# Kernel tuning notes

Measured on AMD Instinct MI355X. Metric: run time of the kernel, lower is better.

The kernel has to match this reference:

```python
import math
import jax, jax.numpy as jnp
import numpy as np

TOP_K = 16
LOW_FREQ = 1
MAX_SEL = 32


def setup_inputs() -> dict:
    key = jax.random.key(0)
    x = jax.random.normal(key, (32, 2048, 512), dtype=jnp.float32)
    return {"x": x}


def reference(x):
    # x: (B, T, D)
    B, T, D = x.shape
    dtype = x.dtype

    xf = jnp.fft.rfft(x, axis=1)  # (B, T//2+1, D) complex
    f_full = jnp.fft.rfftfreq(T, d=1.0).astype(dtype)
    if T % 2 == 0:
        xf = xf[:, LOW_FREQ:-1, :]
        f_vec = f_full[LOW_FREQ:-1]
    else:
        xf = xf[:, LOW_FREQ:, :]
        f_vec = f_full[LOW_FREQ:]
    Lf = xf.shape[1]
    K = min(TOP_K, Lf)

    # top-k over frequency axis, per (b, d)
    xf_t = jnp.transpose(xf, (0, 2, 1))  # (B, D, Lf)
    _, idx = jax.lax.top_k(jnp.abs(xf_t), K)  # (B, D, K), sorted descending
    idx = idx[:, :, : min(MAX_SEL, K)]
    Ksel = idx.shape[2]

    x_sel = jnp.take_along_axis(xf_t, idx, axis=2)  # (B, D, Ksel) complex
    f_sel = f_vec[idx]                               # (B, D, Ksel)
    amp = jnp.abs(x_sel).astype(dtype)
    ph = jnp.angle(x_sel).astype(dtype)

    # y[b,t,d] = sum_k amp * cos(2*pi*f*t + phase), t = linspace(0,1,T)
    two_pi_t = (2.0 * math.pi) * jnp.linspace(0.0, 1.0, T, dtype=dtype)  # (T,)

    def step(acc, kin):
        a, f, p = kin  # each (B, D)
        acc = acc + a[..., None] * jnp.cos(f[..., None] * two_pi_t + p[..., None])
        return acc, None

    init = jnp.zeros((B, D, T), dtype)
    ks = (jnp.moveaxis(amp, 2, 0), jnp.moveaxis(f_sel, 2, 0), jnp.moveaxis(ph, 2, 0))
    y_bdt, _ = jax.lax.scan(step, init, ks)
    return jnp.transpose(y_bdt, (0, 2, 1))  # (B, T, D)
```

## Files before the change

kernel.cpp:

```cpp
#include <hip/hip_runtime.h>
#include <math.h>

#ifndef M_PI
#define M_PI 3.14159265358979323846
#endif

constexpr int cB = 32;
constexpr int cT = 2048;
constexpr int cD = 512;
constexpr int cK = 16;
constexpr int TCH = 64;

__device__ __forceinline__ int PZ(int i) { return i + (i >> 4); }

__device__ __forceinline__ float2 twLO(const float2* TW, int e) {
  return TW[PZ(e)];
}
__device__ __forceinline__ float2 twHI(const float2* TW, int e) {
  float2 w = TW[PZ(e - 512)];
  return make_float2(w.y, -w.x);
}
__device__ __forceinline__ float2 twDYN(const float2* TW, int e) {
  float2 w = TW[PZ(e & 511)];
  return (e < 512) ? w : make_float2(w.y, -w.x);
}

__global__ __launch_bounds__(256) void k_transpose(const float* __restrict__ x,
                                                   float* __restrict__ xt) {
  __shared__ float tile[64][65];
  const int b  = blockIdx.z;
  const int t0 = blockIdx.y * 64;
  const int d0 = blockIdx.x * 64;
  const int tid = threadIdx.x;
  const int r = tid >> 4;
  const int c = tid & 15;

  const float4* x4 = (const float4*)(x + ((size_t)b * cT + t0) * cD + d0);
#pragma unroll
  for (int u = 0; u < 4; ++u) {
    const int row = r + 16 * u;
    const float4 v = x4[row * (cD / 4) + c];
    tile[row][4 * c + 0] = v.x;
    tile[row][4 * c + 1] = v.y;
    tile[row][4 * c + 2] = v.z;
    tile[row][4 * c + 3] = v.w;
  }
  __syncthreads();
  float* xtp = xt + ((size_t)b * cD + d0) * cT + t0;
#pragma unroll
  for (int u = 0; u < 4; ++u) {
    const int dr = r + 16 * u;
    float4 o;
    o.x = tile[4 * c + 0][dr];
    o.y = tile[4 * c + 1][dr];
    o.z = tile[4 * c + 2][dr];
    o.w = tile[4 * c + 3][dr];
    ((float4*)(xtp + (size_t)dr * cT))[c] = o;
  }
}

template <int S>
__device__ __forceinline__ void pass8(float2* Z, const float2* TW, int B0, int O) {
  float vr[8], vi[8];
#pragma unroll
  for (int m = 0; m < 8; ++m) {
    const float2 z = Z[PZ(B0 + S * m)];
    vr[m] = z.x; vi[m] = z.y;
  }
  constexpr int E1 = 1024 / (4 * S);
  constexpr int E2 = 1024 / (2 * S);
  constexpr int E3 = 1024 / S;
#pragma unroll
  for (int m = 0; m < 4; ++m) {
    const int e = (O + S * m) * E1;
    const float2 w = (m < 2) ? twLO(TW, e) : twHI(TW, e);
    const float ar = vr[m], ai = vi[m], br = vr[m + 4], bi = vi[m + 4];
    vr[m] = ar + br; vi[m] = ai + bi;
    const float tr = ar - br, ti = ai - bi;
    vr[m + 4] = tr * w.x - ti * w.y; vi[m + 4] = tr * w.y + ti * w.x;
  }
#pragma unroll
  for (int q = 0; q < 8; q += 4) {
#pragma unroll
    for (int m2 = 0; m2 < 2; ++m2) {
      const int m = q + m2;
      const int e = (O + S * m2) * E2;
      const float2 w = (m2 == 0) ? twLO(TW, e) : twHI(TW, e);
      const float ar = vr[m], ai = vi[m], br = vr[m + 2], bi = vi[m + 2];
      vr[m] = ar + br; vi[m] = ai + bi;
      const float tr = ar - br, ti = ai - bi;
      vr[m + 2] = tr * w.x - ti * w.y; vi[m + 2] = tr * w.y + ti * w.x;
    }
  }
  {
    const int e = O * E3;
    const float2 w = (S == 1) ? twLO(TW, 0) : twDYN(TW, e);
#pragma unroll
    for (int m = 0; m < 8; m += 2) {
      const float ar = vr[m], ai = vi[m], br = vr[m + 1], bi = vi[m + 1];
      vr[m] = ar + br; vi[m] = ai + bi;
      const float tr = ar - br, ti = ai - bi;
      vr[m + 1] = tr * w.x - ti * w.y; vi[m + 1] = tr * w.y + ti * w.x;
    }
  }
#pragma unroll
  for (int m = 0; m < 8; ++m) Z[PZ(B0 + S * m)] = make_float2(vr[m], vi[m]);
}

__global__ __launch_bounds__(256) void k_fft_topk(const float* __restrict__ xt,
                                                  float* __restrict__ amp_out,
                                                  float* __restrict__ kf_out,
                                                  float* __restrict__ ph_out) {
  __shared__ float2 Z[2176];
  __shared__ float2 TW[544];
  __shared__ float  CV[128];
  __shared__ int    CK[128];
  __shared__ int    CC[4];

  const int tid   = threadIdx.x;
  const int lane  = tid & 63;
  const int wave  = tid >> 6;
  const int blk   = blockIdx.x;
  const int b     = blk >> 8;
  const int dpair = blk & 255;
  const int d0    = dpair * 2;

  const float* colA = xt + ((size_t)b * cD + d0) * cT;
  const float* colB = colA + cT;

  for (int j = tid; j < 512; j += 256) {
    float s, c;
    __sincosf(-2.0f * (float)M_PI * (float)j * (1.0f / 2048.0f), &s, &c);
    TW[PZ(j)] = make_float2(c, s);
  }
  const float4* a4 = (const float4*)colA;
  const float4* b4 = (const float4*)colB;
#pragma unroll
  for (int u = 0; u < 2; ++u) {
    const int i4 = tid + 256 * u;
    const float4 va = a4[i4];
    const float4 vb = b4[i4];
    const int base = i4 * 4;
    Z[PZ(base + 0)] = make_float2(va.x, vb.x);
    Z[PZ(base + 1)] = make_float2(va.y, vb.y);
    Z[PZ(base + 2)] = make_float2(va.z, vb.z);
    Z[PZ(base + 3)] = make_float2(va.w, vb.w);
  }
  __syncthreads();

#pragma unroll
  for (int u = 0; u < 2; ++u) {
    const int O = tid + 256 * u;
    float vr[4], vi[4];
#pragma unroll
    for (int m = 0; m < 4; ++m) {
      const float2 z = Z[PZ(O + 512 * m)];
      vr[m] = z.x; vi[m] = z.y;
    }
#pragma unroll
    for (int m = 0; m < 2; ++m) {
      const float2 w = (m == 0) ? twLO(TW, O) : twHI(TW, O + 512);
      const float ar = vr[m], ai = vi[m], br = vr[m + 2], bi = vi[m + 2];
      vr[m] = ar + br; vi[m] = ai + bi;
      const float tr = ar - br, ti = ai - bi;
      vr[m + 2] = tr * w.x - ti * w.y; vi[m + 2] = tr * w.y + ti * w.x;
    }
    {
      const float2 w = (u == 0) ? twLO(TW, 2 * O) : twHI(TW, 2 * O);
#pragma unroll
      for (int m = 0; m < 4; m += 2) {
        const float ar = vr[m], ai = vi[m], br = vr[m + 1], bi = vi[m + 1];
        vr[m] = ar + br; vi[m] = ai + bi;
        const float tr = ar - br, ti = ai - bi;
        vr[m + 1] = tr * w.x - ti * w.y; vi[m + 1] = tr * w.y + ti * w.x;
      }
    }
#pragma unroll
    for (int m = 0; m < 4; ++m) Z[PZ(O + 512 * m)] = make_float2(vr[m], vi[m]);
  }
  __syncthreads();

  pass8<64>(Z, TW, (tid >> 6) * 512 + (tid & 63), tid & 63);
  __syncthreads();
  pass8<8>(Z, TW, (tid >> 3) * 64 + (tid & 7), tid & 7);
  __syncthreads();
  pass8<1>(Z, TW, tid * 8, 0);
  __syncthreads();

  const int col  = wave >> 1;
  const int half = wave & 1;
  float v[8];
  int   kk[8];
#pragma unroll
  for (int u = 0; u < 8; ++u) {
    const int k = half * 512 + lane + 64 * u;
    kk[u] = k;
    if (k == 0) { v[u] = -1.0f; continue; }
    const float2 p = Z[PZ((int)(__brev((unsigned)k) >> 21))];
    const float2 q = Z[PZ((int)(__brev((unsigned)(2048 - k)) >> 21))];
    float xr, xi;
    if (col == 0) { xr = p.x + q.x; xi = p.y - q.y; }
    else          { xr = p.y + q.y; xi = q.x - p.x; }
    v[u] = xr * xr + xi * xi;
  }

  {
    float lm = v[0];
#pragma unroll
    for (int j = 1; j < 8; ++j) lm = fmaxf(lm, v[j]);
    float sm = lm;
#pragma unroll
    for (int k2 = 2; k2 <= 64; k2 <<= 1) {
#pragma unroll
      for (int j = k2 >> 1; j > 0; j >>= 1) {
        const float om = __shfl_xor(sm, j);
        const bool wmin = ((lane & k2) == 0) != ((lane & j) == 0);
        const bool oless = (om < sm);
        sm = (oless == wmin) ? om : sm;
      }
    }
    const float thr = __shfl(sm, 16);

    unsigned long long mball[8];
    int cnt = 0;
#pragma unroll
    for (int j = 0; j < 8; ++j) {
      mball[j] = __ballot(v[j] >= thr);
      cnt += __popcll(mball[j]);
    }

    if (cnt <= 32) {
      int pos = 0;
#pragma unroll
      for (int j = 0; j < 8; ++j) {
        const int p = pos + __popcll(mball[j] & ((1ull << lane) - 1ull));
        if (v[j] >= thr) { CV[wave * 32 + p] = v[j]; CK[wave * 32 + p] = kk[j]; }
        pos += __popcll(mball[j]);
      }
      if (lane == 0) CC[wave] = cnt;
    } else {
      float fv[8];
#pragma unroll
      for (int j = 0; j < 8; ++j) fv[j] = v[j];
      for (int it = 0; it < cK + 1; ++it) {
        float bv = fv[0]; int bj = 0;
#pragma unroll
        for (int j = 1; j < 8; ++j) if (fv[j] > bv) { bv = fv[j]; bj = j; }
        int bk = kk[bj];
        for (int off = 32; off > 0; off >>= 1) {
          const float ov = __shfl_down(bv, off);
          const int   ok = __shfl_down(bk, off);
          if (ov > bv) { bv = ov; bk = ok; }
        }
        const int   bkb = __shfl(bk, 0);
        const float bvb = __shfl(bv, 0);
#pragma unroll
        for (int j = 0; j < 8; ++j) if (kk[j] == bkb) fv[j] = -1.0f;
        if (lane == 0) { CV[wave * 32 + it] = bvb; CK[wave * 32 + it] = bkb; }
      }
      if (lane == 0) CC[wave] = cK + 1;
    }
  }
  __syncthreads();

  if ((wave & 1) == 0) {
    const int c0 = CC[wave];
    const int c1 = CC[wave + 1];
    const int n  = c0 + c1;
    float mv = -1.0f;
    int   mk = 5000 + lane;
    if (lane < c0)     { mv = CV[wave * 32 + lane];            mk = CK[wave * 32 + lane]; }
    else if (lane < n) { mv = CV[(wave + 1) * 32 + lane - c0]; mk = CK[(wave + 1) * 32 + lane - c0]; }

#pragma unroll
    for (int k2 = 2; k2 <= 64; k2 <<= 1) {
#pragma unroll
      for (int j = k2 >> 1; j > 0; j >>= 1) {
        const float ov = __shfl_xor(mv, j);
        const int   ok = __shfl_xor(mk, j);
        const bool wmin  = ((lane & k2) == 0) != ((lane & j) == 0);
        const bool oless = (ov < mv) || (ov == mv && ok > mk);
        if (oless == wmin) { mv = ov; mk = ok; }
      }
    }
    const float myv = mv;
    const int   myk = mk;

    const float v15 = __shfl(myv, 15);
    const float v16 = __shfl(myv, 16);
    const int   k15 = __shfl(myk, 15);
    const int   k16 = __shfl(myk, 16);
    bool  do_swap = false;
    double aR = 0.0, pR = 0.0;
    if (v15 - v16 < 1e-3f * v15) {
      const float* colp = col ? colB : colA;
      double m2[2], XR[2], XI[2];
      for (int bb = 0; bb < 2; ++bb) {
        const int k = bb ? k16 : k15;
        double sr = 0.0, si = 0.0;
        for (int u = 0; u < 32; ++u) {
          const int t = lane + 64 * u;
          const int m = (k * t) & 2047;
          double s, c;
          sincos(-M_PI * (double)m / 1024.0, &s, &c);
          const double xv = (double)colp[t];
          sr += xv * c; si += xv * s;
        }
        for (int off = 32; off > 0; off >>= 1) {
          sr += __shfl_down(sr, off);
          si += __shfl_down(si, off);
        }
        sr = __shfl(sr, 0); si = __shfl(si, 0);
        m2[bb] = sr * sr + si * si; XR[bb] = sr; XI[bb] = si;
      }
      if (m2[1] > m2[0]) {
        do_swap = true;
        aR = sqrt(m2[1]);
        pR = atan2(XI[1], XR[1]);
      }
    }

    if (lane < cK) {
      float a, p, kf;
      if (do_swap && lane == 15) {
        a = (float)aR; p = (float)pR; kf = (float)k16;
      } else {
        const int k = myk;
        const float2 zp = Z[PZ((int)(__brev((unsigned)k) >> 21))];
        const float2 zq = Z[PZ((int)(__brev((unsigned)(2048 - k)) >> 21))];
        float xr, xi;
        if (col == 0) { xr = 0.5f * (zp.x + zq.x); xi = 0.5f * (zp.y - zq.y); }
        else          { xr = 0.5f * (zp.y + zq.y); xi = 0.5f * (zq.x - zp.x); }
        a = sqrtf(xr * xr + xi * xi);
        p = atan2f(xi, xr);
        kf = (float)k;
      }
      const size_t cidx = ((size_t)b * cD + (d0 + col)) * cK + lane;
      amp_out[cidx] = a;
      kf_out[cidx]  = kf;
      ph_out[cidx]  = p;
    }
  }
}

__global__ __launch_bounds__(256) void k_recon(const float* __restrict__ amp_in,
                                               const float* __restrict__ kf_in,
                                               const float* __restrict__ ph_in,
                                               float* __restrict__ y) {
  const int tid = threadIdx.x;
  const int d   = blockIdx.y * 256 + tid;
  const int b   = blockIdx.z;
  const int t0  = blockIdx.x * TCH;
  const size_t cidx = ((size_t)b * cD + d) * cK;
  const float Cw = (float)(2.0 * M_PI / (2047.0 * 2048.0));
  const float t0f = (float)t0;

  float amp[cK], kf[cK], ph[cK];
#pragma unroll
  for (int q = 0; q < 4; ++q) {
    const float4 va = ((const float4*)(amp_in + cidx))[q];
    const float4 vk = ((const float4*)(kf_in + cidx))[q];
    const float4 vp = ((const float4*)(ph_in + cidx))[q];
    amp[4*q+0] = va.x; amp[4*q+1] = va.y; amp[4*q+2] = va.z; amp[4*q+3] = va.w;
    kf [4*q+0] = vk.x; kf [4*q+1] = vk.y; kf [4*q+2] = vk.z; kf [4*q+3] = vk.w;
    ph [4*q+0] = vp.x; ph [4*q+1] = vp.y; ph [4*q+2] = vp.z; ph [4*q+3] = vp.w;
  }

  float r[cK], dd[cK], cm[cK];
  float acc0 = 0.0f, acc1 = 0.0f;
#pragma unroll
  for (int j = 0; j < cK; ++j) {
    const float w  = kf[j] * Cw;
    const float w2 = w * w;
    cm[j] = w2 - w2 * w2 * (1.0f / 12.0f);
    const float kt = kf[j] * t0f;
    const float r0 = amp[j] * __cosf(__fmaf_rn(kt, Cw, ph[j]));
    const float r1 = amp[j] * __cosf(__fmaf_rn(kt + kf[j], Cw, ph[j]));
    r[j] = r1; dd[j] = r1 - r0;
    acc0 += r0; acc1 += r1;
  }
  float* yp = y + ((size_t)b * cT + t0) * cD + d;
  yp[0] = acc0;
  yp[cD] = acc1;
  yp += 2 * (size_t)cD;
#pragma unroll 2
  for (int t = 2; t < TCH; ++t) {
    float acc = 0.0f;
#pragma unroll
    for (int j = 0; j < cK; ++j) {
      dd[j] = __fmaf_rn(-cm[j], r[j], dd[j]);
      r[j] += dd[j];
      acc += r[j];
    }
    *yp = acc;
    yp += cD;
  }
}

extern "C" void kernel_launch(void* const* d_in, const int* in_sizes, int n_in,
                              void* d_out, int out_size, void* d_ws, size_t ws_size,
                              hipStream_t stream) {
  const float* x = (const float*)d_in[0];
  float* out = (float*)d_out;
  float* xt = out;

  float* amp = (float*)d_ws;
  float* kf  = amp + (size_t)cB * cD * cK;
  float* ph  = kf + (size_t)cB * cD * cK;

  dim3 g1(cD / 64, cT / 64, cB), b1(256, 1, 1);
  k_transpose<<<g1, b1, 0, stream>>>(x, xt);

  k_fft_topk<<<cB * cD / 2, 256, 0, stream>>>(xt, amp, kf, ph);

  dim3 g3(cT / TCH, cD / 256, cB), b3(256, 1, 1);
  k_recon<<<g3, b3, 0, stream>>>(amp, kf, ph, out);
}
```

Before: 365.5 us.

## Drop transpose kernel and load strided columns directly in FFT kernel

Removes the separate transpose pass: the FFT/top-k kernel now reads each column pair directly from x as strided float2 loads. The block index is swizzled so that consecutive blocks read neighbouring d-pairs within the same batch, aiming to share cache lines across blocks through L2/MALL. This removes one full read and one full write of the input tensor, plus a kernel launch. The cost is uncoalesced 8-byte strided global reads, which depend on cache reuse across concurrently running blocks. The rare double-precision refinement path also now reads with a stride.

Measured after the change: 334.5 us. 1.09x faster.

```diff
diff --git a/kernel.cpp b/kernel.cpp
--- a/kernel.cpp
+++ b/kernel.cpp
@@ -23,40 +23,6 @@
 __device__ __forceinline__ float2 twDYN(const float2* TW, int e) {
   float2 w = TW[PZ(e & 511)];
   return (e < 512) ? w : make_float2(w.y, -w.x);
-}
-
-__global__ __launch_bounds__(256) void k_transpose(const float* __restrict__ x,
-                                                   float* __restrict__ xt) {
-  __shared__ float tile[64][65];
-  const int b  = blockIdx.z;
-  const int t0 = blockIdx.y * 64;
-  const int d0 = blockIdx.x * 64;
-  const int tid = threadIdx.x;
-  const int r = tid >> 4;
-  const int c = tid & 15;
-
-  const float4* x4 = (const float4*)(x + ((size_t)b * cT + t0) * cD + d0);
-#pragma unroll
-  for (int u = 0; u < 4; ++u) {
-    const int row = r + 16 * u;
-    const float4 v = x4[row * (cD / 4) + c];
-    tile[row][4 * c + 0] = v.x;
-    tile[row][4 * c + 1] = v.y;
-    tile[row][4 * c + 2] = v.z;
-    tile[row][4 * c + 3] = v.w;
-  }
-  __syncthreads();
-  float* xtp = xt + ((size_t)b * cD + d0) * cT + t0;
-#pragma unroll
-  for (int u = 0; u < 4; ++u) {
-    const int dr = r + 16 * u;
-    float4 o;
-    o.x = tile[4 * c + 0][dr];
-    o.y = tile[4 * c + 1][dr];
-    o.z = tile[4 * c + 2][dr];
-    o.w = tile[4 * c + 3][dr];
-    ((float4*)(xtp + (size_t)dr * cT))[c] = o;
-  }
 }
 
 template <int S>
@@ -107,7 +73,7 @@
   for (int m = 0; m < 8; ++m) Z[PZ(B0 + S * m)] = make_float2(vr[m], vi[m]);
 }
 
-__global__ __launch_bounds__(256) void k_fft_topk(const float* __restrict__ xt,
+__global__ __launch_bounds__(256) void k_fft_topk(const float* __restrict__ x,
                                                   float* __restrict__ amp_out,
                                                   float* __restrict__ kf_out,
                                                   float* __restrict__ ph_out) {
@@ -120,31 +86,31 @@
   const int tid   = threadIdx.x;
   const int lane  = tid & 63;
   const int wave  = tid >> 6;
-  const int blk   = blockIdx.x;
-  const int b     = blk >> 8;
-  const int dpair = blk & 255;
+
+  const int i_  = blockIdx.x;
+  const int c_  = i_ & 7;
+  const int j_  = i_ >> 3;
+  const int G_  = c_ * 64 + (j_ >> 4);
+  const int s_  = j_ & 15;
+  const int b     = G_ >> 4;
+  const int dpair = ((G_ & 15) << 4) | s_;
   const int d0    = dpair * 2;
 
-  const float* colA = xt + ((size_t)b * cD + d0) * cT;
-  const float* colB = colA + cT;
+  const float2* xp = (const float2*)x + (size_t)b * cT * (cD / 2) + dpair;
+  float2 vv[8];
+#pragma unroll
+  for (int u = 0; u < 8; ++u) {
+    vv[u] = xp[(size_t)(tid + 256 * u) * (cD / 2)];
+  }
 
   for (int j = tid; j < 512; j += 256) {
     float s, c;
     __sincosf(-2.0f * (float)M_PI * (float)j * (1.0f / 2048.0f), &s, &c);
     TW[PZ(j)] = make_float2(c, s);
   }
-  const float4* a4 = (const float4*)colA;
-  const float4* b4 = (const float4*)colB;
-#pragma unroll
-  for (int u = 0; u < 2; ++u) {
-    const int i4 = tid + 256 * u;
-    const float4 va = a4[i4];
-    const float4 vb = b4[i4];
-    const int base = i4 * 4;
-    Z[PZ(base + 0)] = make_float2(va.x, vb.x);
-    Z[PZ(base + 1)] = make_float2(va.y, vb.y);
-    Z[PZ(base + 2)] = make_float2(va.z, vb.z);
-    Z[PZ(base + 3)] = make_float2(va.w, vb.w);
+#pragma unroll
+  for (int u = 0; u < 8; ++u) {
+    Z[PZ(tid + 256 * u)] = vv[u];
   }
   __syncthreads();
 
@@ -293,7 +259,7 @@
     bool  do_swap = false;
     double aR = 0.0, pR = 0.0;
     if (v15 - v16 < 1e-3f * v15) {
-      const float* colp = col ? colB : colA;
+      const float* colp = x + (size_t)b * cT * cD + (d0 + col);
       double m2[2], XR[2], XI[2];
       for (int bb = 0; bb < 2; ++bb) {
         const int k = bb ? k16 : k15;
@@ -303,7 +269,7 @@
           const int m = (k * t) & 2047;
           double s, c;
           sincos(-M_PI * (double)m / 1024.0, &s, &c);
-          const double xv = (double)colp[t];
+          const double xv = (double)colp[(size_t)t * cD];
           sr += xv * c; si += xv * s;
         }
         for (int off = 32; off > 0; off >>= 1) {
@@ -402,16 +368,12 @@
                               hipStream_t stream) {
   const float* x = (const float*)d_in[0];
   float* out = (float*)d_out;
-  float* xt = out;
 
   float* amp = (float*)d_ws;
   float* kf  = amp + (size_t)cB * cD * cK;
   float* ph  = kf + (size_t)cB * cD * cK;
 
-  dim3 g1(cD / 64, cT / 64, cB), b1(256, 1, 1);
-  k_transpose<<<g1, b1, 0, stream>>>(x, xt);
-
-  k_fft_topk<<<cB * cD / 2, 256, 0, stream>>>(xt, amp, kf, ph);
+  k_fft_topk<<<cB * cD / 2, 256, 0, stream>>>(x, amp, kf, ph);
 
   dim3 g3(cT / TCH, cD / 256, cB), b3(256, 1, 1);
   k_recon<<<g3, b3, 0, stream>>>(amp, kf, ph, out);
```
